# Performance work log

Measured on AMD Instinct MI355X. Metric: run time of the kernel, lower is better.

## Reference

```python
import jax, jax.numpy as jnp
import numpy as np

N_TOKENS = 32768
DIM = 2048
N_EXPERTS = 64
TOP_K = 8
N_GROUP = 8
TOPK_GROUP = 4
ROUTE_SCALE = 2.5
EPS = 1e-20


def setup_inputs() -> dict:
    key = jax.random.key(0)
    k1, k2 = jax.random.split(key)
    hidden_states = jax.random.normal(k1, (N_TOKENS, DIM), dtype=jnp.float32)
    weight = jax.random.normal(k2, (N_EXPERTS, DIM), dtype=jnp.float32) * 0.02
    e_score_correction_bias = jnp.zeros((N_EXPERTS,), dtype=jnp.float32)
    return {"hidden_states": hidden_states, "weight": weight,
            "e_score_correction_bias": e_score_correction_bias}


def reference(hidden_states, weight, e_score_correction_bias):
    # router logits in fp32: [N, E]
    logits = jnp.einsum('nd,ed->ne', hidden_states.astype(jnp.float32),
                        weight.astype(jnp.float32))
    scores = jax.nn.sigmoid(logits)  # score_func == 'sigmoid'

    # --- top-k index selection (no-grad path in torch) ---
    sfc = scores + e_score_correction_bias[None, :]  # [N, E]
    per_group = N_EXPERTS // N_GROUP
    # group score = sum of top-2 scores within each group: [N, G]
    grouped = sfc.reshape(-1, N_GROUP, per_group)
    group_scores = jax.lax.top_k(grouped, 2)[0].sum(axis=-1)
    # pick top `TOPK_GROUP` groups
    _, group_idx = jax.lax.top_k(group_scores, TOPK_GROUP)  # [N, topk_group]
    n = group_scores.shape[0]
    group_mask = jnp.zeros_like(group_scores).at[
        jnp.arange(n)[:, None], group_idx].set(1.0)  # [N, G]
    score_mask = jnp.repeat(group_mask, per_group, axis=1)  # [N, E]
    masked_scores = jnp.where(score_mask > 0, sfc, 0.0)
    _, topk_indices = jax.lax.top_k(masked_scores, TOP_K)  # [N, top_k]

    # gather weights from *unbiased* scores, normalize, scale
    topk_weights = jnp.take_along_axis(scores, topk_indices, axis=1)
    denom = topk_weights.sum(axis=-1, keepdims=True) + EPS
    topk_weights = topk_weights / denom * ROUTE_SCALE
    return topk_indices, topk_weights
```

## Files before the change

### kernel.cpp

```cpp
#include <hip/hip_runtime.h>
#include <math.h>

#define NT 32768
#define DIM 2048
#define NE 64
#define RSCALE 2.5f
#define REPS 1e-20f
#define KC 32
#define NCH (DIM / KC)
#define TOK 64

#define HL_BUF 12288
#define WL_OFF 24576
#define BS_OFF 49152
#define ARENA 49408

typedef const __attribute__((address_space(1))) void GV;
typedef __attribute__((address_space(3))) void LV;
typedef __attribute__((ext_vector_type(8))) short short8x;
typedef __attribute__((ext_vector_type(4))) float f32x4;
typedef __attribute__((ext_vector_type(4))) unsigned int uint4x;

__device__ __align__(16) char WImg[NCH][3 * 4096];

#define PACKHI(odd, even) __builtin_amdgcn_perm((odd), (even), 0x07060302u)

__device__ __forceinline__ void decomp4(f32x4 x, unsigned int o[6]) {
    unsigned int u0 = __float_as_uint(x.x), u1 = __float_as_uint(x.y);
    unsigned int u2 = __float_as_uint(x.z), u3 = __float_as_uint(x.w);
    o[0] = PACKHI(u1, u0); o[1] = PACKHI(u3, u2);
    float r0 = x.x - __uint_as_float(u0 & 0xffff0000u);
    float r1 = x.y - __uint_as_float(u1 & 0xffff0000u);
    float r2 = x.z - __uint_as_float(u2 & 0xffff0000u);
    float r3 = x.w - __uint_as_float(u3 & 0xffff0000u);
    unsigned int v0 = __float_as_uint(r0), v1 = __float_as_uint(r1);
    unsigned int v2 = __float_as_uint(r2), v3 = __float_as_uint(r3);
    o[2] = PACKHI(v1, v0); o[3] = PACKHI(v3, v2);
    float s0 = r0 - __uint_as_float(v0 & 0xffff0000u);
    float s1 = r1 - __uint_as_float(v1 & 0xffff0000u);
    float s2 = r2 - __uint_as_float(v2 & 0xffff0000u);
    float s3 = r3 - __uint_as_float(v3 & 0xffff0000u);
    o[4] = PACKHI(__float_as_uint(s1), __float_as_uint(s0));
    o[5] = PACKHI(__float_as_uint(s3), __float_as_uint(s2));
}

__device__ __forceinline__ void decomp8(f32x4 a, f32x4 b,
                                        short8x* f0, short8x* f1, short8x* f2) {
    unsigned int oa[6], ob[6];
    decomp4(a, oa); decomp4(b, ob);
    uint4x t0 = {oa[0], oa[1], ob[0], ob[1]};
    uint4x t1 = {oa[2], oa[3], ob[2], ob[3]};
    uint4x t2 = {oa[4], oa[5], ob[4], ob[5]};
    *f0 = __builtin_bit_cast(short8x, t0);
    *f1 = __builtin_bit_cast(short8x, t1);
    *f2 = __builtin_bit_cast(short8x, t2);
}

__global__ void prep_w_kernel(const float* __restrict__ W) {
    const int ch = blockIdx.x;
    const int tid = threadIdx.x;
    const int srow = tid >> 2;
    const int sq   = tid & 3;
    const float* src = W + (size_t)srow * DIM + ch * KC + sq * 8;
    f32x4 lo = *(const f32x4*)src;
    f32x4 hi = *(const f32x4*)(src + 4);
    short8x f0, f1, f2;
    decomp8(lo, hi, &f0, &f1, &f2);
    const int soff = srow * 64 + ((sq ^ ((srow >> 1) & 3)) << 4);
    *(short8x*)&WImg[ch][0 * 4096 + soff] = f0;
    *(short8x*)&WImg[ch][1 * 4096 + soff] = f1;
    *(short8x*)&WImg[ch][2 * 4096 + soff] = f2;
}

#define STAGE_ISSUE(HA, HB, KOFF) do { \
    HA = *(const f32x4*)(hgsrc + (KOFF)); \
    HB = *(const f32x4*)(hgsrc + (KOFF) + 4); \
} while (0)

#define STAGE_WRITE_H(HA, HB, PN) do { \
    short8x f0_, f1_, f2_; \
    decomp8(HA, HB, &f0_, &f1_, &f2_); \
    *(short8x*)(arena + (PN) * HL_BUF + 0 * 4096 + soff) = f0_; \
    *(short8x*)(arena + (PN) * HL_BUF + 1 * 4096 + soff) = f1_; \
    *(short8x*)(arena + (PN) * HL_BUF + 2 * 4096 + soff) = f2_; \
} while (0)

#define WSTAGE(CHN, PN) do { \
    const char* ws_ = WImg[(CHN)]; \
    __builtin_amdgcn_global_load_lds((GV*)(ws_ + 0 * 4096 + wgofs), \
        (LV*)(arena + WL_OFF + (PN) * HL_BUF + 0 * 4096 + wlofs), 16, 0, 0); \
    __builtin_amdgcn_global_load_lds((GV*)(ws_ + 1 * 4096 + wgofs), \
        (LV*)(arena + WL_OFF + (PN) * HL_BUF + 1 * 4096 + wlofs), 16, 0, 0); \
    __builtin_amdgcn_global_load_lds((GV*)(ws_ + 2 * 4096 + wgofs), \
        (LV*)(arena + WL_OFF + (PN) * HL_BUF + 2 * 4096 + wlofs), 16, 0, 0); \
} while (0)

#define COMPUTE(P) do { \
    const char* hb = arena + (P) * HL_BUF; \
    const char* wb = arena + WL_OFF + (P) * HL_BUF; \
    short8x a0[2], a1[2], a2[2]; \
    _Pragma("unroll") \
    for (int tt = 0; tt < 2; ++tt) { \
        const int t_ = wr * 32 + tt * 16 + l15; \
        const int ro_ = t_ * 64 + ((g ^ ((t_ >> 1) & 3)) << 4); \
        a0[tt] = *(const short8x*)(hb + 0 * 4096 + ro_); \
        a1[tt] = *(const short8x*)(hb + 1 * 4096 + ro_); \
        a2[tt] = *(const short8x*)(hb + 2 * 4096 + ro_); \
    } \
    _Pragma("unroll") \
    for (int et = 0; et < 2; ++et) { \
        const int e_ = wc * 32 + et * 16 + l15; \
        const int ro_ = e_ * 64 + ((g ^ ((e_ >> 1) & 3)) << 4); \
        short8x b0 = *(const short8x*)(wb + 0 * 4096 + ro_); \
        short8x b1 = *(const short8x*)(wb + 1 * 4096 + ro_); \
        short8x b2 = *(const short8x*)(wb + 2 * 4096 + ro_); \
        _Pragma("unroll") \
        for (int tt = 0; tt < 2; ++tt) { \
            Cm[tt][et] = __builtin_amdgcn_mfma_f32_16x16x32_bf16(a0[tt], b0, Cm[tt][et], 0, 0, 0); \
            Cc[tt][et] = __builtin_amdgcn_mfma_f32_16x16x32_bf16(a1[tt], b0, Cc[tt][et], 0, 0, 0); \
            Cc[tt][et] = __builtin_amdgcn_mfma_f32_16x16x32_bf16(a2[tt], b0, Cc[tt][et], 0, 0, 0); \
            Cc[tt][et] = __builtin_amdgcn_mfma_f32_16x16x32_bf16(a0[tt], b1, Cc[tt][et], 0, 0, 0); \
            Cc[tt][et] = __builtin_amdgcn_mfma_f32_16x16x32_bf16(a1[tt], b1, Cc[tt][et], 0, 0, 0); \
            Cc[tt][et] = __builtin_amdgcn_mfma_f32_16x16x32_bf16(a0[tt], b2, Cc[tt][et], 0, 0, 0); \
        } \
    } \
} while (0)

#define DRAIN do { \
    _Pragma("unroll") \
    for (int tt = 0; tt < 2; ++tt) \
        _Pragma("unroll") \
        for (int et = 0; et < 2; ++et) { \
            _Pragma("unroll") \
            for (int r = 0; r < 4; ++r) \
                md[tt][et][r] += (double)Cm[tt][et][r] + (double)Cc[tt][et][r]; \
            Cm[tt][et] = (f32x4)0.0f; Cc[tt][et] = (f32x4)0.0f; \
        } \
} while (0)

__global__ __launch_bounds__(256, 2) void router_kernel(
    const float* __restrict__ H,
    const float* __restrict__ B,
    float* __restrict__ out)
{
    __shared__ __align__(16) char arena[ARENA];
    float* bsf = (float*)(arena + BS_OFF);
    float* scf = (float*)(arena);

    const int tid  = threadIdx.x;
    const int lane = tid & 63;
    const int w    = __builtin_amdgcn_readfirstlane(tid >> 6);
    const int l15  = lane & 15, g = lane >> 4;
    const size_t tb = (size_t)blockIdx.x * TOK;

    if (tid < NE) bsf[tid] = B[tid];

    const int srow = tid >> 2;
    const int sq   = tid & 3;
    const float* hgsrc = H + (tb + (size_t)srow) * DIM + sq * 8;
    const int soff = srow * 64 + ((sq ^ ((srow >> 1) & 3)) << 4);

    const int wgofs = tid * 16;
    const int wlofs = w * 1024;

    const int wr = w & 1, wc = w >> 1;

    f32x4 Cm[2][2], Cc[2][2];
    double md[2][2][4];
    #pragma unroll
    for (int tt = 0; tt < 2; ++tt)
        #pragma unroll
        for (int et = 0; et < 2; ++et) {
            Cm[tt][et] = (f32x4)0.0f; Cc[tt][et] = (f32x4)0.0f;
            #pragma unroll
            for (int r = 0; r < 4; ++r) md[tt][et][r] = 0.0;
        }

    f32x4 hA0, hA1, hB0, hB1;

    WSTAGE(0, 0);
    STAGE_ISSUE(hA0, hA1, 0);
    STAGE_WRITE_H(hA0, hA1, 0);
    STAGE_ISSUE(hB0, hB1, KC);
    __syncthreads();

    for (int chb = 0; chb < NCH; chb += 2) {
        WSTAGE(chb + 1, 1);
        if (chb + 2 < NCH) STAGE_ISSUE(hA0, hA1, (chb + 2) * KC);
        COMPUTE(0);
        STAGE_WRITE_H(hB0, hB1, 1);
        __syncthreads();

        if (chb + 2 < NCH) {
            WSTAGE(chb + 2, 0);
            STAGE_ISSUE(hB0, hB1, (chb + 3 < NCH) ? (chb + 3) * KC : (chb + 2) * KC);
        }
        COMPUTE(1);
        if (chb + 2 < NCH) STAGE_WRITE_H(hA0, hA1, 0);
        if (((chb + 1) & 7) == 7) DRAIN;
        __syncthreads();
    }

    #pragma unroll
    for (int tt = 0; tt < 2; ++tt)
        #pragma unroll
        for (int et = 0; et < 2; ++et)
            #pragma unroll
            for (int r = 0; r < 4; ++r) {
                float logit = (float)md[tt][et][r];
                float s = 1.0f / (1.0f + expf(-logit));
                int t = wr * 32 + tt * 16 + g * 4 + r;
                int e = wc * 32 + et * 16 + l15;
                scf[t * 65 + e] = s;
            }
    __syncthreads();

    if ((tid & 3) == 0) {
        const int t = tid >> 2;
        const float* sc = &scf[t * 65];
        float gs[8];
        #pragma unroll
        for (int gg = 0; gg < 8; ++gg) {
            float m1 = -1e30f, m2 = -1e30f;
            #pragma unroll
            for (int j = 0; j < 8; ++j) {
                float v = sc[gg * 8 + j] + bsf[gg * 8 + j];
                if (v > m1) { m2 = m1; m1 = v; }
                else if (v > m2) { m2 = v; }
            }
            gs[gg] = m1 + m2;
        }
        unsigned gmask = 0;
        for (int i = 0; i < 4; ++i) {
            float best = -1e30f; int bg = 0;
            for (int gg = 0; gg < 8; ++gg)
                if (!((gmask >> gg) & 1u) && gs[gg] > best) { best = gs[gg]; bg = gg; }
            gmask |= 1u << bg;
        }
        unsigned long long picked = 0ull;
        int   idxs[8];
        float wts[8];
        float wsum = 0.0f;
        for (int i = 0; i < 8; ++i) {
            float best = -1e30f; int bi = 0;
            for (int e = 0; e < 64; ++e) {
                if ((picked >> e) & 1ull) continue;
                float v = ((gmask >> (e >> 3)) & 1u) ? (sc[e] + bsf[e]) : 0.0f;
                if (v > best) { best = v; bi = e; }
            }
            picked |= 1ull << bi;
            idxs[i] = bi;
            wts[i] = sc[bi];
            wsum += sc[bi];
        }
        const float scale = RSCALE / (wsum + REPS);
        const size_t token = tb + t;
        #pragma unroll
        for (int i = 0; i < 8; ++i) {
            out[token * 8 + i] = (float)idxs[i];
            out[(size_t)NT * 8 + token * 8 + i] = wts[i] * scale;
        }
    }
}

extern "C" void kernel_launch(void* const* d_in, const int* in_sizes, int n_in,
                              void* d_out, int out_size, void* d_ws, size_t ws_size,
                              hipStream_t stream) {
    (void)in_sizes; (void)n_in; (void)out_size; (void)d_ws; (void)ws_size;
    const float* H = (const float*)d_in[0];
    const float* W = (const float*)d_in[1];
    const float* B = (const float*)d_in[2];
    float* out = (float*)d_out;
    prep_w_kernel<<<dim3(NCH), dim3(256), 0, stream>>>(W);
    router_kernel<<<dim3(NT / TOK), dim3(256), 0, stream>>>(H, B, out);
}
```

Baseline: 123.6 us.

## Halve tokens per block to shrink LDS and registers for higher occupancy

Cuts the tile from 64 to 32 tokens per block. Each wave now holds one token sub-tile instead of two, and only half the threads stage hidden-state rows. LDS and accumulator register use shrink, so launch bounds rise to 4 blocks per CU for better latency hiding. In exchange the grid doubles and every weight chunk is reloaded by twice as many blocks. Each weight fragment also feeds fewer MFMAs, so LDS reads per flop go up.

```diff
diff --git a/kernel.cpp b/kernel.cpp
--- a/kernel.cpp
+++ b/kernel.cpp
@@ -8,12 +8,13 @@
 #define REPS 1e-20f
 #define KC 32
 #define NCH (DIM / KC)
-#define TOK 64
-
-#define HL_BUF 12288
-#define WL_OFF 24576
-#define BS_OFF 49152
-#define ARENA 49408
+#define TOK 32
+
+#define HL_BUF 6144
+#define WL_OFF 12288
+#define WL_BUF 12288
+#define BS_OFF 36864
+#define ARENA 37120
 
 typedef const __attribute__((address_space(1))) void GV;
 typedef __attribute__((address_space(3))) void LV;
@@ -73,40 +74,41 @@
 }
 
 #define STAGE_ISSUE(HA, HB, KOFF) do { \
-    HA = *(const f32x4*)(hgsrc + (KOFF)); \
-    HB = *(const f32x4*)(hgsrc + (KOFF) + 4); \
+    if (hact) { \
+        HA = *(const f32x4*)(hgsrc + (KOFF)); \
+        HB = *(const f32x4*)(hgsrc + (KOFF) + 4); \
+    } \
 } while (0)
 
 #define STAGE_WRITE_H(HA, HB, PN) do { \
-    short8x f0_, f1_, f2_; \
-    decomp8(HA, HB, &f0_, &f1_, &f2_); \
-    *(short8x*)(arena + (PN) * HL_BUF + 0 * 4096 + soff) = f0_; \
-    *(short8x*)(arena + (PN) * HL_BUF + 1 * 4096 + soff) = f1_; \
-    *(short8x*)(arena + (PN) * HL_BUF + 2 * 4096 + soff) = f2_; \
+    if (hact) { \
+        short8x f0_, f1_, f2_; \
+        decomp8(HA, HB, &f0_, &f1_, &f2_); \
+        *(short8x*)(arena + (PN) * HL_BUF + 0 * 2048 + soff) = f0_; \
+        *(short8x*)(arena + (PN) * HL_BUF + 1 * 2048 + soff) = f1_; \
+        *(short8x*)(arena + (PN) * HL_BUF + 2 * 2048 + soff) = f2_; \
+    } \
 } while (0)
 
 #define WSTAGE(CHN, PN) do { \
     const char* ws_ = WImg[(CHN)]; \
     __builtin_amdgcn_global_load_lds((GV*)(ws_ + 0 * 4096 + wgofs), \
-        (LV*)(arena + WL_OFF + (PN) * HL_BUF + 0 * 4096 + wlofs), 16, 0, 0); \
+        (LV*)(arena + WL_OFF + (PN) * WL_BUF + 0 * 4096 + wlofs), 16, 0, 0); \
     __builtin_amdgcn_global_load_lds((GV*)(ws_ + 1 * 4096 + wgofs), \
-        (LV*)(arena + WL_OFF + (PN) * HL_BUF + 1 * 4096 + wlofs), 16, 0, 0); \
+        (LV*)(arena + WL_OFF + (PN) * WL_BUF + 1 * 4096 + wlofs), 16, 0, 0); \
     __builtin_amdgcn_global_load_lds((GV*)(ws_ + 2 * 4096 + wgofs), \
-        (LV*)(arena + WL_OFF + (PN) * HL_BUF + 2 * 4096 + wlofs), 16, 0, 0); \
+        (LV*)(arena + WL_OFF + (PN) * WL_BUF + 2 * 4096 + wlofs), 16, 0, 0); \
 } while (0)
 
 #define COMPUTE(P) do { \
     const char* hb = arena + (P) * HL_BUF; \
-    const char* wb = arena + WL_OFF + (P) * HL_BUF; \
-    short8x a0[2], a1[2], a2[2]; \
-    _Pragma("unroll") \
-    for (int tt = 0; tt < 2; ++tt) { \
-        const int t_ = wr * 32 + tt * 16 + l15; \
-        const int ro_ = t_ * 64 + ((g ^ ((t_ >> 1) & 3)) << 4); \
-        a0[tt] = *(const short8x*)(hb + 0 * 4096 + ro_); \
-        a1[tt] = *(const short8x*)(hb + 1 * 4096 + ro_); \
-        a2[tt] = *(const short8x*)(hb + 2 * 4096 + ro_); \
-    } \
+    const char* wb = arena + WL_OFF + (P) * WL_BUF; \
+    short8x a0, a1, a2; \
+    { const int t_ = wr * 16 + l15; \
+      const int ro_ = t_ * 64 + ((g ^ ((t_ >> 1) & 3)) << 4); \
+      a0 = *(const short8x*)(hb + 0 * 2048 + ro_); \
+      a1 = *(const short8x*)(hb + 1 * 2048 + ro_); \
+      a2 = *(const short8x*)(hb + 2 * 2048 + ro_); } \
     _Pragma("unroll") \
     for (int et = 0; et < 2; ++et) { \
         const int e_ = wc * 32 + et * 16 + l15; \
@@ -114,31 +116,26 @@
         short8x b0 = *(const short8x*)(wb + 0 * 4096 + ro_); \
         short8x b1 = *(const short8x*)(wb + 1 * 4096 + ro_); \
         short8x b2 = *(const short8x*)(wb + 2 * 4096 + ro_); \
-        _Pragma("unroll") \
-        for (int tt = 0; tt < 2; ++tt) { \
-            Cm[tt][et] = __builtin_amdgcn_mfma_f32_16x16x32_bf16(a0[tt], b0, Cm[tt][et], 0, 0, 0); \
-            Cc[tt][et] = __builtin_amdgcn_mfma_f32_16x16x32_bf16(a1[tt], b0, Cc[tt][et], 0, 0, 0); \
-            Cc[tt][et] = __builtin_amdgcn_mfma_f32_16x16x32_bf16(a2[tt], b0, Cc[tt][et], 0, 0, 0); \
-            Cc[tt][et] = __builtin_amdgcn_mfma_f32_16x16x32_bf16(a0[tt], b1, Cc[tt][et], 0, 0, 0); \
-            Cc[tt][et] = __builtin_amdgcn_mfma_f32_16x16x32_bf16(a1[tt], b1, Cc[tt][et], 0, 0, 0); \
-            Cc[tt][et] = __builtin_amdgcn_mfma_f32_16x16x32_bf16(a0[tt], b2, Cc[tt][et], 0, 0, 0); \
-        } \
+        Cm[et] = __builtin_amdgcn_mfma_f32_16x16x32_bf16(a0, b0, Cm[et], 0, 0, 0); \
+        Cc[et] = __builtin_amdgcn_mfma_f32_16x16x32_bf16(a1, b0, Cc[et], 0, 0, 0); \
+        Cc[et] = __builtin_amdgcn_mfma_f32_16x16x32_bf16(a2, b0, Cc[et], 0, 0, 0); \
+        Cc[et] = __builtin_amdgcn_mfma_f32_16x16x32_bf16(a0, b1, Cc[et], 0, 0, 0); \
+        Cc[et] = __builtin_amdgcn_mfma_f32_16x16x32_bf16(a1, b1, Cc[et], 0, 0, 0); \
+        Cc[et] = __builtin_amdgcn_mfma_f32_16x16x32_bf16(a0, b2, Cc[et], 0, 0, 0); \
     } \
 } while (0)
 
 #define DRAIN do { \
     _Pragma("unroll") \
-    for (int tt = 0; tt < 2; ++tt) \
+    for (int et = 0; et < 2; ++et) { \
         _Pragma("unroll") \
-        for (int et = 0; et < 2; ++et) { \
-            _Pragma("unroll") \
-            for (int r = 0; r < 4; ++r) \
-                md[tt][et][r] += (double)Cm[tt][et][r] + (double)Cc[tt][et][r]; \
-            Cm[tt][et] = (f32x4)0.0f; Cc[tt][et] = (f32x4)0.0f; \
-        } \
-} while (0)
-
-__global__ __launch_bounds__(256, 2) void router_kernel(
+        for (int r = 0; r < 4; ++r) \
+            md[et][r] += (double)Cm[et][r] + (double)Cc[et][r]; \
+        Cm[et] = (f32x4)0.0f; Cc[et] = (f32x4)0.0f; \
+    } \
+} while (0)
+
+__global__ __launch_bounds__(256, 4) void router_kernel(
     const float* __restrict__ H,
     const float* __restrict__ B,
     float* __restrict__ out)
@@ -155,9 +152,10 @@
 
     if (tid < NE) bsf[tid] = B[tid];
 
+    const bool hact = tid < 128;
     const int srow = tid >> 2;
     const int sq   = tid & 3;
-    const float* hgsrc = H + (tb + (size_t)srow) * DIM + sq * 8;
+    const float* hgsrc = H + (tb + (size_t)(hact ? srow : 0)) * DIM + sq * 8;
     const int soff = srow * 64 + ((sq ^ ((srow >> 1) & 3)) << 4);
 
     const int wgofs = tid * 16;
@@ -165,16 +163,14 @@
 
     const int wr = w & 1, wc = w >> 1;
 
-    f32x4 Cm[2][2], Cc[2][2];
-    double md[2][2][4];
+    f32x4 Cm[2], Cc[2];
+    double md[2][4];
     #pragma unroll
-    for (int tt = 0; tt < 2; ++tt)
-        #pragma unroll
-        for (int et = 0; et < 2; ++et) {
-            Cm[tt][et] = (f32x4)0.0f; Cc[tt][et] = (f32x4)0.0f;
-            #pragma unroll
-            for (int r = 0; r < 4; ++r) md[tt][et][r] = 0.0;
-        }
+    for (int et = 0; et < 2; ++et) {
+        Cm[et] = (f32x4)0.0f; Cc[et] = (f32x4)0.0f;
+        #pragma unroll
+        for (int r = 0; r < 4; ++r) md[et][r] = 0.0;
+    }
 
     f32x4 hA0, hA1, hB0, hB1;
 
@@ -202,21 +198,19 @@
     }
 
     #pragma unroll
-    for (int tt = 0; tt < 2; ++tt)
-        #pragma unroll
-        for (int et = 0; et < 2; ++et)
-            #pragma unroll
-            for (int r = 0; r < 4; ++r) {
-                float logit = (float)md[tt][et][r];
-                float s = 1.0f / (1.0f + expf(-logit));
-                int t = wr * 32 + tt * 16 + g * 4 + r;
-                int e = wc * 32 + et * 16 + l15;
-                scf[t * 65 + e] = s;
-            }
+    for (int et = 0; et < 2; ++et)
+        #pragma unroll
+        for (int r = 0; r < 4; ++r) {
+            float logit = (float)md[et][r];
+            float s = 1.0f / (1.0f + expf(-logit));
+            int t = wr * 16 + g * 4 + r;
+            int e = wc * 32 + et * 16 + l15;
+            scf[t * 65 + e] = s;
+        }
     __syncthreads();
 
-    if ((tid & 3) == 0) {
-        const int t = tid >> 2;
+    if ((tid & 7) == 0) {
+        const int t = tid >> 3;
         const float* sc = &scf[t * 65];
         float gs[8];
         #pragma unroll
```

After: 143.3 us. 15.9% more time.
